# Performance work log

Measured on AMD Instinct MI355X. Metric: run time of the kernel, lower is better.

## Reference

```python
import jax, jax.numpy as jnp
import numpy as np

N_EMBED = 1024
EMBED_DIM = 64
BETA = 0.25


def setup_inputs() -> dict:
    key = jax.random.key(0)
    k1, k2 = jax.random.split(key)
    x = jax.random.normal(k1, (32, EMBED_DIM, 64, 64), dtype=jnp.float32)  # NCHW, C == embed_dim
    embed = jax.random.uniform(
        k2, (N_EMBED, EMBED_DIM), dtype=jnp.float32,
        minval=-1.0 / N_EMBED, maxval=1.0 / N_EMBED,
    )
    return {"x": x, "embed": embed}


def reference(x, embed):
    # NCHW -> NHWC, flatten spatial+batch to rows of embed_dim
    z = jnp.transpose(x, (0, 2, 3, 1))                      # [B,H,W,D]
    zf = z.reshape(-1, EMBED_DIM)                           # [N,D]
    # squared L2 distance to every codeword: ||z||^2 + ||e||^2 - 2 z.e
    dist = (
        jnp.sum(zf * zf, axis=1, keepdims=True)
        + jnp.sum(embed * embed, axis=1)
        - 2.0 * zf @ embed.T
    )                                                       # [N, n_embed]
    idx = jnp.argmin(dist, axis=1)                          # [N]
    # one-hot @ embed == direct gather (same math, no scatter/matmul)
    z_q = embed[idx].reshape(z.shape)                       # [B,H,W,D]
    sg = jax.lax.stop_gradient
    loss = jnp.mean((sg(z_q) - z) ** 2) + BETA * jnp.mean((z_q - sg(z)) ** 2)
    # straight-through estimator
    z_q = z + sg(z_q - z)
    z_q = jnp.transpose(z_q, (0, 3, 1, 2))                  # back to NCHW
    return (z_q, loss)
```

## Files before the change

### kernel.cpp

```cpp
#include <hip/hip_runtime.h>


#define TOTAL_ELEMS 8388608
#define LOSS_SCALE (1.25f / 8388608.f)

typedef float  f32x4  __attribute__((ext_vector_type(4)));
typedef unsigned int u32x4 __attribute__((ext_vector_type(4)));
typedef long   longx2 __attribute__((ext_vector_type(2)));

static __device__ __forceinline__ void gload_lds16(const void* g, void* l) {
    __builtin_amdgcn_global_load_lds(
        (const __attribute__((address_space(1))) void*)g,
        (__attribute__((address_space(3))) void*)l,
        16, 0, 0);
}

static __device__ __forceinline__ unsigned int umax(unsigned int a, unsigned int b) {
    return a > b ? a : b;
}

__global__ void vq_prep(const float* __restrict__ embed,
                        unsigned char* __restrict__ eb,
                        float* __restrict__ c0,
                        float* __restrict__ loss_slot) {
    int t   = blockIdx.x * 256 + threadIdx.x;
    int row = t >> 2, qd = t & 3;
    const float* s0 = embed + row * 64 + qd * 8;
    const float* s1 = embed + row * 64 + 32 + qd * 8;
    f32x4 v0 = *(const f32x4*)s0, v1 = *(const f32x4*)(s0 + 4);
    f32x4 w0 = *(const f32x4*)s1, w1 = *(const f32x4*)(s1 + 4);
    float s = v0[0]*v0[0] + v0[1]*v0[1] + v0[2]*v0[2] + v0[3]*v0[3]
            + v1[0]*v1[0] + v1[1]*v1[1] + v1[2]*v1[2] + v1[3]*v1[3]
            + w0[0]*w0[0] + w0[1]*w0[1] + w0[2]*w0[2] + w0[3]*w0[3]
            + w1[0]*w1[0] + w1[1]*w1[1] + w1[2]*w1[2] + w1[3]*w1[3];
    unsigned int d0 = 0, d1 = 0, d2 = 0, d3 = 0;
    d0 = __builtin_amdgcn_cvt_pk_fp8_f32(v0[0]*1024.f, v0[1]*1024.f, d0, false);
    d0 = __builtin_amdgcn_cvt_pk_fp8_f32(v0[2]*1024.f, v0[3]*1024.f, d0, true);
    d1 = __builtin_amdgcn_cvt_pk_fp8_f32(v1[0]*1024.f, v1[1]*1024.f, d1, false);
    d1 = __builtin_amdgcn_cvt_pk_fp8_f32(v1[2]*1024.f, v1[3]*1024.f, d1, true);
    d2 = __builtin_amdgcn_cvt_pk_fp8_f32(w0[0]*1024.f, w0[1]*1024.f, d2, false);
    d2 = __builtin_amdgcn_cvt_pk_fp8_f32(w0[2]*1024.f, w0[3]*1024.f, d2, true);
    d3 = __builtin_amdgcn_cvt_pk_fp8_f32(w1[0]*1024.f, w1[1]*1024.f, d3, false);
    d3 = __builtin_amdgcn_cvt_pk_fp8_f32(w1[2]*1024.f, w1[3]*1024.f, d3, true);
    u32x4 o = {d0, d1, d2, d3};
    *(u32x4*)((char*)eb + row * 64 + qd * 16) = o;
    s += __shfl_xor(s, 1);
    s += __shfl_xor(s, 2);
    if (qd == 0) c0[row] = 64.f - 512.f * s;
    if (t == 0) *loss_slot = 0.f;
}

__global__ __launch_bounds__(256, 2) void vq_main(
    const float* __restrict__ x,
    const float* __restrict__ embed,
    const unsigned char* __restrict__ eb,
    const float* __restrict__ c0,
    float* __restrict__ out,
    float* __restrict__ loss) {

    __shared__ __align__(16) unsigned char cb[65536];
    __shared__ __align__(16) float c0l[1024];
    __shared__ float lpart[4];

    const int t    = threadIdx.x;
    const int wv   = t >> 6, lane = t & 63;
    const int l15  = lane & 15, lq = lane >> 4;

    const int blk = blockIdx.x;
    const int b   = blk >> 4;
    const int h0  = (blk & 15) * 4;
    const size_t xbase = (size_t)b * 262144 + (size_t)h0 * 64;

    const char* ebp = (const char*)eb;

#pragma unroll
    for (int s = 0; s < 16; s++)
        gload_lds16(ebp + s * 4096 + t * 16, &cb[s * 4096 + t * 16]);

    *(f32x4*)(c0l + t * 4) = *(const f32x4*)(c0 + t * 4);

    float part = 0.f;
    long bfr[4][2];
#pragma unroll
    for (int nt = 0; nt < 4; nt++) {
#pragma unroll
        for (int kh = 0; kh < 2; kh++) {
            unsigned int dw[2];
#pragma unroll
            for (int p = 0; p < 2; p++) {
                float f[4];
#pragma unroll
                for (int j = 0; j < 4; j++) {
                    f[j] = x[xbase + (size_t)(kh * 32 + lq * 8 + p * 4 + j) * 4096
                             + (size_t)wv * 64 + nt * 16 + l15];
                    part += f[j] * f[j];
                }
                unsigned int r = 0;
                r = __builtin_amdgcn_cvt_pk_fp8_f32(f[0], f[1], r, false);
                r = __builtin_amdgcn_cvt_pk_fp8_f32(f[2], f[3], r, true);
                dw[p] = r;
            }
            bfr[nt][kh] = (long)(((unsigned long long)dw[1] << 32) | dw[0]);
        }
    }
    __syncthreads();

    unsigned int key[4] = {0u, 0u, 0u, 0u};
    const unsigned char* abase = &cb[l15 * 64 + lq * 16];
    const float* cbase = c0l + lq * 4;
#pragma unroll 8
    for (int mt = 0; mt < 64; mt++) {
        longx2 av = *(const longx2*)(abase + mt * 1024);
        f32x4 c0v = *(const f32x4*)(cbase + mt * 16);
        const int invm = 1023 - mt * 16 - lq * 4;
#pragma unroll
        for (int nt = 0; nt < 4; nt++) {
            f32x4 acc = __builtin_amdgcn_mfma_f32_16x16x32_fp8_fp8(
                av[0], bfr[nt][0], c0v, 0, 0, 0);
            acc = __builtin_amdgcn_mfma_f32_16x16x32_fp8_fp8(
                av[1], bfr[nt][1], acc, 0, 0, 0);
            unsigned int k0 = (__float_as_uint(acc[0]) & 0xFFFFFC00u) | (unsigned int)(invm);
            unsigned int k1 = (__float_as_uint(acc[1]) & 0xFFFFFC00u) | (unsigned int)(invm - 1);
            unsigned int k2 = (__float_as_uint(acc[2]) & 0xFFFFFC00u) | (unsigned int)(invm - 2);
            unsigned int k3 = (__float_as_uint(acc[3]) & 0xFFFFFC00u) | (unsigned int)(invm - 3);
            key[nt] = umax(key[nt], umax(umax(k0, k1), umax(k2, k3)));
        }
    }

#pragma unroll
    for (int nt = 0; nt < 4; nt++) {
        unsigned int k = key[nt];
        unsigned int o = (unsigned int)__shfl_xor((int)k, 16); k = umax(k, o);
        o = (unsigned int)__shfl_xor((int)k, 32);              k = umax(k, o);
        key[nt] = k;
        part -= (1.f / 2048.f) * __uint_as_float(k & 0xFFFFFC00u);
    }

    unsigned int klo = (lane & 16) ? key[1] : key[0];
    unsigned int khi = (lane & 16) ? key[3] : key[2];
    unsigned int ks  = (lane & 32) ? khi : klo;
    const int idx = 1023 - (int)(ks & 1023u);

#pragma unroll
    for (int off = 1; off < 64; off <<= 1) part += __shfl_xor(part, off);
    if (lane == 0) lpart[wv] = part;

    const float* erow = embed + idx * 64;
    float* orow = out + xbase + (size_t)wv * 64 + lane;
#pragma unroll
    for (int c4 = 0; c4 < 16; c4++) {
        f32x4 ev = *(const f32x4*)(erow + c4 * 4);
#pragma unroll
        for (int j = 0; j < 4; j++)
            orow[(size_t)(c4 * 4 + j) * 4096] = ev[j];
    }

    __syncthreads();
    if (t == 0) {
        atomicAdd(loss, (lpart[0] + lpart[1] + lpart[2] + lpart[3] + 32.0f) * LOSS_SCALE);
    }
}

extern "C" void kernel_launch(void* const* d_in, const int* in_sizes, int n_in,
                              void* d_out, int out_size, void* d_ws, size_t ws_size,
                              hipStream_t stream) {
    const float* x     = (const float*)d_in[0];
    const float* embed = (const float*)d_in[1];
    unsigned char* eb  = (unsigned char*)d_ws;
    float* c0          = (float*)((char*)d_ws + 65536);
    float* out  = (float*)d_out;
    float* loss = out + TOTAL_ELEMS;

    vq_prep<<<16, 256, 0, stream>>>(embed, eb, c0, loss);
    vq_main<<<512, 256, 0, stream>>>(x, embed, eb, c0, out, loss);
}
```

Measured before the change: 37.06 us.

## Split each block's rows over 8 waves and pad codebook LDS rows

Block size goes from 256 to 512 threads, and each wave now handles 32 spatial positions instead of 64. The per-wave MFMA work and register footprint are halved, which allows more waves per CU to hide latency. The fp8 codebook in LDS is repacked with a 72-byte row stride, read as two 8-byte loads per step, to reduce LDS bank conflicts. In exchange, every wave re-reads the full codebook from LDS for half the work, so LDS traffic per output roughly doubles, and LDS per block grows slightly.

After: 35.43 us. 1.05x faster.

```diff
diff --git a/kernel.cpp b/kernel.cpp
--- a/kernel.cpp
+++ b/kernel.cpp
@@ -3,10 +3,9 @@
 
 #define TOTAL_ELEMS 8388608
 #define LOSS_SCALE (1.25f / 8388608.f)
+#define ROWB 72
 
-typedef float  f32x4  __attribute__((ext_vector_type(4)));
-typedef unsigned int u32x4 __attribute__((ext_vector_type(4)));
-typedef long   longx2 __attribute__((ext_vector_type(2)));
+typedef float f32x4 __attribute__((ext_vector_type(4)));
 
 static __device__ __forceinline__ void gload_lds16(const void* g, void* l) {
     __builtin_amdgcn_global_load_lds(
@@ -42,15 +41,18 @@
     d2 = __builtin_amdgcn_cvt_pk_fp8_f32(w0[2]*1024.f, w0[3]*1024.f, d2, true);
     d3 = __builtin_amdgcn_cvt_pk_fp8_f32(w1[0]*1024.f, w1[1]*1024.f, d3, false);
     d3 = __builtin_amdgcn_cvt_pk_fp8_f32(w1[2]*1024.f, w1[3]*1024.f, d3, true);
-    u32x4 o = {d0, d1, d2, d3};
-    *(u32x4*)((char*)eb + row * 64 + qd * 16) = o;
+    unsigned long long g0 = (unsigned long long)d0 | ((unsigned long long)d1 << 32);
+    unsigned long long g1 = (unsigned long long)d2 | ((unsigned long long)d3 << 32);
+    char* rb = (char*)eb + row * ROWB;
+    *(unsigned long long*)(rb + qd * 8)      = g0;
+    *(unsigned long long*)(rb + 32 + qd * 8) = g1;
     s += __shfl_xor(s, 1);
     s += __shfl_xor(s, 2);
     if (qd == 0) c0[row] = 64.f - 512.f * s;
     if (t == 0) *loss_slot = 0.f;
 }
 
-__global__ __launch_bounds__(256, 2) void vq_main(
+__global__ __launch_bounds__(512, 4) void vq_main(
     const float* __restrict__ x,
     const float* __restrict__ embed,
     const unsigned char* __restrict__ eb,
@@ -58,9 +60,9 @@
     float* __restrict__ out,
     float* __restrict__ loss) {
 
-    __shared__ __align__(16) unsigned char cb[65536];
+    __shared__ __align__(16) unsigned char cb[1024 * ROWB];
     __shared__ __align__(16) float c0l[1024];
-    __shared__ float lpart[4];
+    __shared__ float lpart[8];
 
     const int t    = threadIdx.x;
     const int wv   = t >> 6, lane = t & 63;
@@ -70,19 +72,20 @@
     const int b   = blk >> 4;
     const int h0  = (blk & 15) * 4;
     const size_t xbase = (size_t)b * 262144 + (size_t)h0 * 64;
+    const int rowoff = (wv >> 1) * 64 + (wv & 1) * 32;
 
     const char* ebp = (const char*)eb;
 
 #pragma unroll
-    for (int s = 0; s < 16; s++)
-        gload_lds16(ebp + s * 4096 + t * 16, &cb[s * 4096 + t * 16]);
+    for (int s = 0; s < 9; s++)
+        gload_lds16(ebp + s * 8192 + t * 16, &cb[s * 8192 + t * 16]);
 
-    *(f32x4*)(c0l + t * 4) = *(const f32x4*)(c0 + t * 4);
+    if (t < 256) *(f32x4*)(c0l + t * 4) = *(const f32x4*)(c0 + t * 4);
 
     float part = 0.f;
-    long bfr[4][2];
+    long bfr[2][2];
 #pragma unroll
-    for (int nt = 0; nt < 4; nt++) {
+    for (int nt = 0; nt < 2; nt++) {
 #pragma unroll
         for (int kh = 0; kh < 2; kh++) {
             unsigned int dw[2];
@@ -92,7 +95,7 @@
 #pragma unroll
                 for (int j = 0; j < 4; j++) {
                     f[j] = x[xbase + (size_t)(kh * 32 + lq * 8 + p * 4 + j) * 4096
-                             + (size_t)wv * 64 + nt * 16 + l15];
+                             + (size_t)rowoff + nt * 16 + l15];
                     part += f[j] * f[j];
                 }
                 unsigned int r = 0;
@@ -105,20 +108,21 @@
     }
     __syncthreads();
 
-    unsigned int key[4] = {0u, 0u, 0u, 0u};
-    const unsigned char* abase = &cb[l15 * 64 + lq * 16];
+    unsigned int key[2] = {0u, 0u};
+    const unsigned char* bbase = &cb[l15 * ROWB + lq * 8];
     const float* cbase = c0l + lq * 4;
 #pragma unroll 8
     for (int mt = 0; mt < 64; mt++) {
-        longx2 av = *(const longx2*)(abase + mt * 1024);
+        long a0 = *(const long*)(bbase + mt * 16 * ROWB);
+        long a1 = *(const long*)(bbase + mt * 16 * ROWB + 32);
         f32x4 c0v = *(const f32x4*)(cbase + mt * 16);
         const int invm = 1023 - mt * 16 - lq * 4;
 #pragma unroll
-        for (int nt = 0; nt < 4; nt++) {
+        for (int nt = 0; nt < 2; nt++) {
             f32x4 acc = __builtin_amdgcn_mfma_f32_16x16x32_fp8_fp8(
-                av[0], bfr[nt][0], c0v, 0, 0, 0);
+                a0, bfr[nt][0], c0v, 0, 0, 0);
             acc = __builtin_amdgcn_mfma_f32_16x16x32_fp8_fp8(
-                av[1], bfr[nt][1], acc, 0, 0, 0);
+                a1, bfr[nt][1], acc, 0, 0, 0);
             unsigned int k0 = (__float_as_uint(acc[0]) & 0xFFFFFC00u) | (unsigned int)(invm);
             unsigned int k1 = (__float_as_uint(acc[1]) & 0xFFFFFC00u) | (unsigned int)(invm - 1);
             unsigned int k2 = (__float_as_uint(acc[2]) & 0xFFFFFC00u) | (unsigned int)(invm - 2);
@@ -128,7 +132,7 @@
     }
 
 #pragma unroll
-    for (int nt = 0; nt < 4; nt++) {
+    for (int nt = 0; nt < 2; nt++) {
         unsigned int k = key[nt];
         unsigned int o = (unsigned int)__shfl_xor((int)k, 16); k = umax(k, o);
         o = (unsigned int)__shfl_xor((int)k, 32);              k = umax(k, o);
@@ -136,19 +140,19 @@
         part -= (1.f / 2048.f) * __uint_as_float(k & 0xFFFFFC00u);
     }
 
-    unsigned int klo = (lane & 16) ? key[1] : key[0];
-    unsigned int khi = (lane & 16) ? key[3] : key[2];
-    unsigned int ks  = (lane & 32) ? khi : klo;
+    unsigned int ks = ((lane >> 4) & 1) ? key[1] : key[0];
     const int idx = 1023 - (int)(ks & 1023u);
 
 #pragma unroll
     for (int off = 1; off < 64; off <<= 1) part += __shfl_xor(part, off);
     if (lane == 0) lpart[wv] = part;
 
-    const float* erow = embed + idx * 64;
-    float* orow = out + xbase + (size_t)wv * 64 + lane;
+    const int ch0 = (lane >> 5) * 32;
+    const int pos = lane & 31;
+    const float* erow = embed + idx * 64 + ch0;
+    float* orow = out + xbase + (size_t)rowoff + pos + (size_t)ch0 * 4096;
 #pragma unroll
-    for (int c4 = 0; c4 < 16; c4++) {
+    for (int c4 = 0; c4 < 8; c4++) {
         f32x4 ev = *(const f32x4*)(erow + c4 * 4);
 #pragma unroll
         for (int j = 0; j < 4; j++)
@@ -157,7 +161,9 @@
 
     __syncthreads();
     if (t == 0) {
-        atomicAdd(loss, (lpart[0] + lpart[1] + lpart[2] + lpart[3] + 32.0f) * LOSS_SCALE);
+        float s = lpart[0] + lpart[1] + lpart[2] + lpart[3]
+                + lpart[4] + lpart[5] + lpart[6] + lpart[7];
+        atomicAdd(loss, (s + 32.0f) * LOSS_SCALE);
     }
 }
 
@@ -167,10 +173,10 @@
     const float* x     = (const float*)d_in[0];
     const float* embed = (const float*)d_in[1];
     unsigned char* eb  = (unsigned char*)d_ws;
-    float* c0          = (float*)((char*)d_ws + 65536);
+    float* c0          = (float*)((char*)d_ws + 73728);
     float* out  = (float*)d_out;
     float* loss = out + TOTAL_ELEMS;
 
     vq_prep<<<16, 256, 0, stream>>>(embed, eb, c0, loss);
-    vq_main<<<512, 256, 0, stream>>>(x, embed, eb, c0, out, loss);
+    vq_main<<<512, 512, 0, stream>>>(x, embed, eb, c0, out, loss);
 }
```
